# Performance work log

Measured on AMD Instinct MI355X. Metric: run time of the kernel, lower is better.

The kernel has to match this reference:

```python
import jax, jax.numpy as jnp
import numpy as np

PAD_ID = 1
NEG = jnp.float32(-1e30)


def setup_inputs() -> dict:
    key = jax.random.key(0)
    ks = jax.random.split(key, 12)
    T, B, S, D, E, V = 20, 32, 400, 512, 512, 50000
    s = 0.02  # weight init scale for numerical sanity
    return {
        "inputs": jax.random.randint(ks[0], (T, B), 0, V),
        "src": jax.random.randint(ks[1], (S, B, 1), 0, V),
        "h_e": jax.random.normal(ks[2], (S, B, D), jnp.float32),
        "h0": jnp.zeros((B, D), jnp.float32),
        "c0": jnp.zeros((B, D), jnp.float32),
        "W_emb": jax.random.normal(ks[3], (V, E), jnp.float32) * s,
        "W_proj": jax.random.normal(ks[4], (E, 3 * D), jnp.float32) * s,
        "b_out": jax.random.normal(ks[5], (V,), jnp.float32) * s,
        "proj_u_W": jax.random.normal(ks[6], (1, 3 * D), jnp.float32) * s,
        "proj_u_b": jnp.zeros((1,), jnp.float32),
        "enc_W": jax.random.normal(ks[7], (D, D), jnp.float32) * s,
        "dec_W": jax.random.normal(ks[8], (D, D), jnp.float32) * s,
        "W_ih": jax.random.normal(ks[9], (4 * D, E), jnp.float32) * s,
        "W_hh": jax.random.normal(ks[10], (4 * D, D), jnp.float32) * s,
        "b_ih": jnp.zeros((4 * D,), jnp.float32),
        "b_hh": jnp.zeros((4 * D,), jnp.float32),
    }


def reference(inputs, src, h_e, h0, c0, W_emb, W_proj, b_out, proj_u_W,
              proj_u_b, enc_W, dec_W, W_ih, W_hh, b_ih, b_hh):
    T, B = inputs.shape
    D = h0.shape[1]
    V = W_emb.shape[0]
    src_bs = src[:, :, 0].T                       # [B, S]
    # Sect 2.4 shared output weights: W_out = tanh(W_emb @ W_proj)  [V, 3D]
    W_out = jnp.tanh(W_emb @ W_proj)
    rows = jnp.arange(B)[:, None]
    tpos = jnp.arange(T)

    def step(carry, xs):
        h, c, hist = carry                        # hist: [T, B, D] decoder-state history
        inp_t, t = xs
        emb = W_emb[inp_t]                        # [B, E]
        # single-layer LSTM cell (torch gate order i, f, g, o)
        gates = emb @ W_ih.T + h @ W_hh.T + b_ih + b_hh
        i, f, g, o = jnp.split(gates, 4, axis=-1)
        c_new = jax.nn.sigmoid(f) * c + jax.nn.sigmoid(i) * jnp.tanh(g)
        hd = jax.nn.sigmoid(o) * jnp.tanh(c_new)  # [B, D]
        # encoder intra-attention
        q = hd @ enc_W.T
        ae = jax.nn.softmax(jnp.einsum('bd,sbd->bs', q, h_e), axis=-1)  # [B, S]
        ce = jnp.einsum('bs,sbd->bd', ae, h_e)
        # decoder intra-attention over steps < t (zero context at t==0)
        qd = hd @ dec_W.T
        sd = jnp.einsum('bd,tbd->bt', qd, hist)
        sd = jnp.where(tpos[None, :] < t, sd, NEG)
        ad = jax.nn.softmax(sd, axis=-1)
        cd = jnp.where(t > 0, jnp.einsum('bt,tbd->bd', ad, hist), 0.0)
        hist = hist.at[t].set(hd)
        # pointer-generator
        ccat = jnp.concatenate([hd, ce, cd], axis=-1)        # [B, 3D]
        logits = ccat @ W_out.T + b_out                      # [B, V]
        logits = logits.at[:, PAD_ID].set(NEG)
        p_gen = jax.nn.softmax(logits, axis=-1)
        p_switch = jax.nn.sigmoid(ccat @ proj_u_W.T + proj_u_b)  # [B, 1]
        # copy distribution: scatter attention into vocab
        copy = jnp.zeros((B, V), logits.dtype).at[rows, src_bs].add(ae)
        scores = copy * p_switch + p_gen * (1.0 - p_switch)
        return (hd, c_new, hist), scores

    hist0 = jnp.zeros((T, B, D), h0.dtype)
    _, scores = jax.lax.scan(step, (h0, c0, hist0), (inputs, tpos))
    return scores  # [T, B, V]
```

## Files before the change

kernel.cpp:

```cpp
#include <hip/hip_runtime.h>
#include <stdint.h>

typedef unsigned short u16;
typedef unsigned int   u32;

using f32x4 = __attribute__((ext_vector_type(4))) float;
using s16x8 = __attribute__((ext_vector_type(8))) short;

#define TT 20
#define BB 32
#define SS 400
#define DD 512
#define VV 50000
#define VP2 50176

__device__ __forceinline__ float bf2f(u16 u){
  u32 x = ((u32)u) << 16;
  return __builtin_bit_cast(float, x);
}
__device__ __forceinline__ u16 f2bf(float f){
  u32 x = __builtin_bit_cast(u32, f);
  x = x + 0x7fffu + ((x >> 16) & 1u);
  return (u16)(x >> 16);
}
__device__ __forceinline__ float sigm(float x){ return 1.0f/(1.0f + __expf(-x)); }
__device__ __forceinline__ float tanh_fast(float x){
  float a = fabsf(x);
  if (a < 0.25f){ float x2 = x*x; return x + x*x2*(-0.33333334f + 0.13333334f*x2); }
  return tanhf(x);
}
__device__ __forceinline__ void gld16(const void* g, void* l){
  __builtin_amdgcn_global_load_lds((const __attribute__((address_space(1))) void*)g,
                                   (__attribute__((address_space(3))) void*)l, 16, 0, 0);
}

__global__ __launch_bounds__(256) void k_prep(
    const float* __restrict__ W_proj,
    const float* __restrict__ W_ih,   const float* __restrict__ W_hh,
    const float* __restrict__ b_ih,   const float* __restrict__ b_hh,
    const float* __restrict__ h0,     const float* __restrict__ c0,
    const float* __restrict__ enc_W,  const float* __restrict__ dec_W,
    const float* __restrict__ W_emb,  const float* __restrict__ h_e,
    const int*   __restrict__ inputs,
    u16* __restrict__ WpT,
    u16* __restrict__ Wihs, u16* __restrict__ Whhs,
    u16* __restrict__ encWb, u16* __restrict__ decWb, float* __restrict__ bgs,
    float* __restrict__ hist, u16* __restrict__ histb, float* __restrict__ c_st,
    float* __restrict__ psE,
    u16* __restrict__ Wembb, u16* __restrict__ heb, u16* __restrict__ emba)
{
  int i = blockIdx.x*256 + threadIdx.x;
  if (i < 1280){ psE[i] = 0.0f; return; }
  i -= 1280;
  if (i < 2048){ int d = i >> 2, g = i & 3; bgs[i] = b_ih[g*512 + d] + b_hh[g*512 + d]; return; }
  i -= 2048;
  if (i < 16384){ float hv = h0[i]; hist[i] = hv; histb[i] = f2bf(hv); c_st[i] = c0[i]; return; }
  i -= 16384;
  if (i < 786432){ int j = i >> 9, k = i & 511; WpT[i] = f2bf(W_proj[k*1536 + j]); return; }
  i -= 786432;
  if (i < 1048576){
    int mp = i >> 9, k = i & 511; int d = mp >> 2, g = mp & 3;
    Wihs[i] = f2bf(W_ih[(size_t)(g*512 + d)*512 + k]); return; }
  i -= 1048576;
  if (i < 1048576){
    int mp = i >> 9, k = i & 511; int d = mp >> 2, g = mp & 3;
    Whhs[i] = f2bf(W_hh[(size_t)(g*512 + d)*512 + k]); return; }
  i -= 1048576;
  if (i < 262144){ encWb[i] = f2bf(enc_W[i]); return; }
  i -= 262144;
  if (i < 262144){ decWb[i] = f2bf(dec_W[i]); return; }
  i -= 262144;
  if (i < 6422528){
    int base = i*4;
    uint2 o;
    if (base < VV*DD){
      float4 v = *(const float4*)&W_emb[base];
      o.x = (u32)f2bf(v.x) | ((u32)f2bf(v.y) << 16);
      o.y = (u32)f2bf(v.z) | ((u32)f2bf(v.w) << 16);
    } else { o.x = 0u; o.y = 0u; }
    *(uint2*)&Wembb[base] = o;
    return; }
  i -= 6422528;
  if (i < 1638400){
    int base = i*4;
    const int s = base >> 14;
    const int b = (base >> 9) & 31;
    const int d = base & 511;
    float4 v = *(const float4*)&h_e[base];
    uint2 o;
    o.x = (u32)f2bf(v.x) | ((u32)f2bf(v.y) << 16);
    o.y = (u32)f2bf(v.z) | ((u32)f2bf(v.w) << 16);
    *(uint2*)&heb[((size_t)(b*SS + s) << 9) + d] = o;
    return; }
  i -= 1638400;
  if (i < 81920){
    int base = i*4;
    int r = base >> 9, k = base & 511;
    float4 v = *(const float4*)&W_emb[(size_t)inputs[r]*DD + k];
    uint2 o;
    o.x = (u32)f2bf(v.x) | ((u32)f2bf(v.y) << 16);
    o.y = (u32)f2bf(v.z) | ((u32)f2bf(v.w) << 16);
    *(uint2*)&emba[base] = o;
    return; }
}

template<int EPI>
__device__ __forceinline__ void gemm_tile(
    const u16* __restrict__ A, const u16* __restrict__ B,
    float* __restrict__ Cf, u16* __restrict__ Cb, const float* __restrict__ bias,
    int K, int mt, int nt, int ldc, int nmax, char* smemc)
{
  u16* As = (u16*)smemc;
  u16* Bs = (u16*)(smemc + 16384);
  const int tid = threadIdx.x;
  const int w = tid >> 6, l = tid & 63;
  const int m0 = mt*128, n0 = nt*128;
  const int srow = tid >> 3;
  const int scol = ((tid & 7) ^ ((tid >> 3) & 7)) * 8;
  const int wm = (w >> 1)*64, wn = (w & 1)*64;
  const int fr = l & 15;
  const int g4 = l >> 4;
  float bv[4];
  if constexpr (EPI == 3){
    #pragma unroll
    for (int j = 0; j < 4; ++j){
      const int c = n0 + wn + j*16 + fr;
      bv[j] = (c < nmax) ? bias[c] : 0.0f;
    }
  }
  f32x4 acc[4][4] = {};
  for (int k0 = 0; k0 < K; k0 += 64){
    #pragma unroll
    for (int j = 0; j < 4; ++j){
      gld16(A + (size_t)(m0 + j*32 + srow)*K + k0 + scol, (char*)As + j*4096 + (w << 10));
      gld16(B + (size_t)(n0 + j*32 + srow)*K + k0 + scol, (char*)Bs + j*4096 + (w << 10));
    }
    __syncthreads();
    #pragma unroll
    for (int h = 0; h < 2; ++h){
      s16x8 af[4], bfr[4];
      #pragma unroll
      for (int i = 0; i < 4; ++i){
        const int ra = wm + i*16 + fr;
        af[i]  = *(const s16x8*)((char*)As + ra*128 + ((((h << 2) + g4) ^ (ra & 7)) << 4));
        const int rb = wn + i*16 + fr;
        bfr[i] = *(const s16x8*)((char*)Bs + rb*128 + ((((h << 2) + g4) ^ (rb & 7)) << 4));
      }
      #pragma unroll
      for (int i = 0; i < 4; ++i)
        #pragma unroll
        for (int j2 = 0; j2 < 4; ++j2)
          acc[i][j2] = __builtin_amdgcn_mfma_f32_16x16x32_bf16(af[i], bfr[j2], acc[i][j2], 0, 0, 0);
    }
    __syncthreads();
  }
  if constexpr (EPI == 0){
    #pragma unroll
    for (int i = 0; i < 4; ++i)
      #pragma unroll
      for (int j = 0; j < 4; ++j)
        #pragma unroll
        for (int r = 0; r < 4; ++r){
          const int row = m0 + wm + i*16 + (l >> 4)*4 + r;
          const int col = n0 + wn + j*16 + fr;
          Cf[(size_t)row*ldc + col] = acc[i][j][r];
        }
  } else {
    u16* Rs = (u16*)smemc;
    #pragma unroll
    for (int i = 0; i < 4; ++i){
      #pragma unroll
      for (int j = 0; j < 4; ++j){
        #pragma unroll
        for (int r = 0; r < 4; ++r){
          const int rl = wm + i*16 + (l >> 4)*4 + r;
          const int cl = wn + j*16 + fr;
          const float v = acc[i][j][r];
          u16 o;
          if constexpr (EPI == 1) o = f2bf(tanh_fast(v));
          else                    o = f2bf(v + bv[j]);
          Rs[rl*136 + cl] = o;
        }
      }
    }
    __syncthreads();
    const int rr0 = tid >> 4;
    const int cb  = (tid & 15)*8;
    #pragma unroll
    for (int p = 0; p < 8; ++p){
      const int row = p*16 + rr0;
      const int gc  = n0 + cb;
      s16x8 val = *(const s16x8*)&Rs[row*136 + cb];
      u16* dst = Cb + (size_t)(m0 + row)*ldc + gc;
      if (EPI == 1 || gc + 8 <= nmax){
        *(s16x8*)dst = val;
      } else {
        #pragma unroll
        for (int q = 0; q < 8; ++q)
          if (gc + q < nmax) dst[q] = (u16)val[q];
      }
    }
  }
}

template<int EPI, int ORD>
__global__ __launch_bounds__(256) void gemm_bt(
    const u16* __restrict__ A, const u16* __restrict__ B,
    float* __restrict__ Cf, u16* __restrict__ Cb, const float* __restrict__ bias,
    int K, int TM, int TN, int ldc, int nmax)
{
  __shared__ __align__(16) char smem[34816];
  int bid = blockIdx.x;
  if (ORD >= 1){
    const int n = TM*TN, x = bid & 7, i = bid >> 3;
    const int q = n >> 3, r = n & 7;
    bid = (x < r ? x*(q+1) : r*(q+1) + (x-r)*q) + i;
  }
  const int mt = (ORD == 1) ? bid / TN : bid % TM;
  const int nt = (ORD == 1) ? bid % TN : bid / TM;
  gemm_tile<EPI>(A, B, Cf, Cb, bias, K, mt, nt, ldc, nmax, smem);
}

__global__ __launch_bounds__(256) void k_lstm(
    const u16* __restrict__ Whhs, const float* __restrict__ X, const float* __restrict__ bgs,
    float* __restrict__ hist, u16* __restrict__ histb, float* __restrict__ c_st,
    u16* __restrict__ ccatb, int t)
{
  __shared__ __align__(16) u16 Hs[32*512];
  __shared__ __align__(16) u16 As[16*512];
  __shared__ float Cp[4][16][32];
  const int blk = blockIdx.x;
  const int tid = threadIdx.x;
  const int w = tid >> 6, l = tid & 63;
  const char* hsrc = (const char*)(histb + (size_t)t*16384);
  #pragma unroll
  for (int p = 0; p < 8; ++p)
    gld16(hsrc + p*4096 + w*1024 + l*16, (char*)Hs + p*4096 + w*1024);
  const char* asrc = (const char*)(Whhs + (size_t)blk*16*512);
  #pragma unroll
  for (int p = 0; p < 4; ++p)
    gld16(asrc + p*4096 + w*1024 + l*16, (char*)As + p*4096 + w*1024);
  __syncthreads();
  {
    const int fr = l & 15, fko = (l >> 4)*8;
    f32x4 acc0 = {}, acc1 = {};
    #pragma unroll
    for (int kk = 0; kk < 4; ++kk){
      const int kb = (w*4 + kk)*32;
      s16x8 af = *(const s16x8*)&As[fr*512 + kb + fko];
      s16x8 b0 = *(const s16x8*)&Hs[fr*512 + kb + fko];
      s16x8 b1 = *(const s16x8*)&Hs[(16 + fr)*512 + kb + fko];
      acc0 = __builtin_amdgcn_mfma_f32_16x16x32_bf16(af, b0, acc0, 0, 0, 0);
      acc1 = __builtin_amdgcn_mfma_f32_16x16x32_bf16(af, b1, acc1, 0, 0, 0);
    }
    #pragma unroll
    for (int r = 0; r < 4; ++r){
      Cp[w][(l >> 4)*4 + r][fr]      = acc0[r];
      Cp[w][(l >> 4)*4 + r][16 + fr] = acc1[r];
    }
  }
  __syncthreads();
  if (tid < 128){
    const int dl = tid >> 5, b = tid & 31;
    const int d = blk*4 + dl;
    const int bd = b*512 + d;
    float gv[4];
    #pragma unroll
    for (int g = 0; g < 4; ++g)
      gv[g] = Cp[0][dl*4 + g][b] + Cp[1][dl*4 + g][b] + Cp[2][dl*4 + g][b] + Cp[3][dl*4 + g][b];
    const float4 x4 = *(const float4*)&X[((size_t)(t*BB + b))*2048 + d*4];
    const float4 g4 = *(const float4*)&bgs[d*4];
    const float iv = gv[0] + x4.x + g4.x;
    const float fv = gv[1] + x4.y + g4.y;
    const float gg = gv[2] + x4.z + g4.z;
    const float ov = gv[3] + x4.w + g4.w;
    const float cn = sigm(fv)*c_st[bd] + sigm(iv)*tanhf(gg);
    const float hd = sigm(ov)*tanhf(cn);
    c_st[bd] = cn;
    hist[(size_t)(t + 1)*16384 + bd] = hd;
    const u16 hb = f2bf(hd);
    histb[(size_t)(t + 1)*16384 + bd] = hb;
    ccatb[((size_t)(t*BB + b))*1536 + d] = hb;
  }
}

__global__ __launch_bounds__(256) void k_bulkq(
    const u16* __restrict__ Hb, const u16* __restrict__ encWb, const u16* __restrict__ decWb,
    float* __restrict__ qe_all, float* __restrict__ qd_all)
{
  __shared__ __align__(16) char smem[34816];
  const int e = blockIdx.x;
  const int which = e / 20;
  const int e2 = e % 20;
  const int mt = e2 % 5, nt = e2 / 5;
  gemm_tile<0>(Hb, which ? decWb : encWb, which ? qd_all : qe_all,
               nullptr, nullptr, 512, mt, nt, 512, 0, smem);
}

__global__ __launch_bounds__(256) void k_attn(
    const u16* __restrict__ heb, const float* __restrict__ hist,
    const float* __restrict__ qe_all, const float* __restrict__ qd_all,
    const float* __restrict__ puW,
    u16* __restrict__ ccatb, float* __restrict__ aeall,
    float* __restrict__ psE, float* __restrict__ psD)
{
  __shared__ float hcur[512];
  __shared__ float qv[512];
  __shared__ float ael[SS];
  __shared__ float red[256];
  __shared__ float part[4*512];
  __shared__ float adl[TT];
  __shared__ float sdl[TT];
  __shared__ float shs[2];
  const int blk = blockIdx.x;
  const int tid = threadIdx.x;

  if (blk < 640){
    const int row = blk;
    const int t = row >> 5, b = row & 31;
    const float* hsrc = hist + (size_t)(t + 1)*16384 + b*512;
    const float* qsrc = qe_all + (size_t)row*512;
    hcur[tid] = hsrc[tid]; hcur[tid + 256] = hsrc[tid + 256];
    qv[tid] = qsrc[tid];   qv[tid + 256] = qsrc[tid + 256];
    __syncthreads();
    for (int pass = 0; pass < 7; ++pass){
      const int s = pass*64 + (tid >> 2);
      if (s < SS){
        const u16* gp = heb + ((size_t)(b*SS + s))*512 + (tid & 3)*128;
        const float* hp = qv + (tid & 3)*128;
        float p = 0.0f;
        #pragma unroll 4
        for (int k8 = 0; k8 < 128; k8 += 8){
          s16x8 g8 = *(const s16x8*)&gp[k8];
          #pragma unroll
          for (int q = 0; q < 8; ++q) p += bf2f((u16)g8[q])*hp[k8 + q];
        }
        p += __shfl_xor(p, 1); p += __shfl_xor(p, 2);
        if ((tid & 3) == 0) ael[s] = p;
      }
    }
    __syncthreads();
    float lm = -1e30f;
    for (int s = tid; s < SS; s += 256) lm = fmaxf(lm, ael[s]);
    red[tid] = lm; __syncthreads();
    for (int st = 128; st; st >>= 1){ if (tid < st) red[tid] = fmaxf(red[tid], red[tid + st]); __syncthreads(); }
    const float M = red[0]; __syncthreads();
    float ls = 0.0f;
    for (int s = tid; s < SS; s += 256){ float p = __expf(ael[s] - M); ael[s] = p; ls += p; }
    red[tid] = ls; __syncthreads();
    for (int st = 128; st; st >>= 1){ if (tid < st) red[tid] += red[tid + st]; __syncthreads(); }
    const float inv = 1.0f/red[0];
    __syncthreads();
    {
      const int g = tid >> 6, th = tid & 63;
      const int d0 = th*8;
      float a8[8] = {};
      for (int s = g; s < SS; s += 4){
        const float a = ael[s];
        s16x8 hv = *(const s16x8*)&heb[((size_t)(b*SS + s))*512 + d0];
        #pragma unroll
        for (int q = 0; q < 8; ++q) a8[q] += a*bf2f((u16)hv[q]);
      }
      *(float4*)&part[g*512 + d0]     = float4{a8[0], a8[1], a8[2], a8[3]};
      *(float4*)&part[g*512 + d0 + 4] = float4{a8[4], a8[5], a8[6], a8[7]};
    }
    __syncthreads();
    {
      const int dd = tid*2;
      float ce0 = part[dd]     + part[512 + dd]     + part[1024 + dd]     + part[1536 + dd];
      float ce1 = part[dd + 1] + part[512 + dd + 1] + part[1024 + dd + 1] + part[1536 + dd + 1];
      ce0 *= inv; ce1 *= inv;
      *(u32*)&ccatb[(size_t)row*1536 + 512 + dd] = (u32)f2bf(ce0) | ((u32)f2bf(ce1) << 16);
      float pv = hcur[dd]*puW[dd] + hcur[dd + 1]*puW[dd + 1]
               + ce0*puW[512 + dd] + ce1*puW[512 + dd + 1];
      red[tid] = pv;
    }
    __syncthreads();
    for (int st = 128; st; st >>= 1){ if (tid < st) red[tid] += red[tid + st]; __syncthreads(); }
    if (tid == 0) psE[row] = red[0];
    for (int s = tid; s < SS; s += 256) aeall[(size_t)row*SS + s] = ael[s]*inv;
  } else {
    const int row = blk - 640;
    const int t = row >> 5, b = row & 31;
    const float* qsrc = qd_all + (size_t)row*512;
    qv[tid] = qsrc[tid]; qv[tid + 256] = qsrc[tid + 256];
    __syncthreads();
    for (int u0 = 0; u0 < t; u0 += 8){
      const int u = u0 + (tid >> 5);
      if (u < t){
        const float* hu = hist + (size_t)(u + 1)*16384 + b*512;
        float p = 0.0f;
        #pragma unroll
        for (int j = 0; j < 4; ++j){
          const int kb = (tid & 31)*4 + j*128;
          const float4 h4 = *(const float4*)&hu[kb];
          const float4 q4 = *(const float4*)&qv[kb];
          p += h4.x*q4.x + h4.y*q4.y + h4.z*q4.z + h4.w*q4.w;
        }
        p += __shfl_xor(p, 1); p += __shfl_xor(p, 2); p += __shfl_xor(p, 4);
        p += __shfl_xor(p, 8); p += __shfl_xor(p, 16);
        if ((tid & 31) == 0) sdl[u] = p;
      }
    }
    __syncthreads();
    if (tid == 0 && t > 0){
      float m2 = -1e30f;
      for (int u = 0; u < t; ++u) m2 = fmaxf(m2, sdl[u]);
      float s2 = 0.0f;
      for (int u = 0; u < t; ++u){ float p = __expf(sdl[u] - m2); adl[u] = p; s2 += p; }
      shs[0] = 1.0f/s2;
    }
    __syncthreads();
    const float invd = (t > 0) ? shs[0] : 0.0f;
    const int d0 = tid*2;
    float e0 = 0.0f, e1 = 0.0f;
    for (int u = 0; u < t; ++u){
      const float a = adl[u];
      const float* hu = hist + (size_t)(u + 1)*16384 + b*512 + d0;
      e0 += a*hu[0]; e1 += a*hu[1];
    }
    e0 *= invd; e1 *= invd;
    *(u32*)&ccatb[(size_t)row*1536 + 1024 + d0] = (u32)f2bf(e0) | ((u32)f2bf(e1) << 16);
    float pv = e0*puW[1024 + d0] + e1*puW[1024 + d0 + 1];
    red[tid] = pv; __syncthreads();
    for (int st = 128; st; st >>= 1){ if (tid < st) red[tid] += red[tid + st]; __syncthreads(); }
    if (tid == 0) psD[row] = red[0];
  }
}

__global__ __launch_bounds__(256) void k_softmax(
    const u16* __restrict__ lg, float* __restrict__ out,
    const float* __restrict__ psE, const float* __restrict__ psD, const float* __restrict__ puB,
    const int* __restrict__ src, const float* __restrict__ ae_all)
{
  const int r = blockIdx.x, tid = threadIdx.x;
  __shared__ float rm[256], rs[256];
  const u16* row = lg + (size_t)r*VP2;
  float m = -1e30f, s = 0.0f;
  for (int v8 = tid*8; v8 < VV; v8 += 2048){
    uint4 pk = *(const uint4*)&row[v8];
    u32 wds[4] = {pk.x, pk.y, pk.z, pk.w};
    #pragma unroll
    for (int q = 0; q < 8; ++q){
      if (v8 + q == 1) continue;
      float x = bf2f((u16)((wds[q >> 1] >> ((q & 1)*16)) & 0xffffu));
      if (x > m){ s = s*__expf(m - x) + 1.0f; m = x; }
      else s += __expf(x - m);
    }
  }
  rm[tid] = m; rs[tid] = s; __syncthreads();
  for (int st = 128; st; st >>= 1){
    if (tid < st){
      float m2 = fmaxf(rm[tid], rm[tid + st]);
      rs[tid] = rs[tid]*__expf(rm[tid] - m2) + rs[tid + st]*__expf(rm[tid + st] - m2);
      rm[tid] = m2;
    }
    __syncthreads();
  }
  const float M = rm[0];
  const float ps = 1.0f/(1.0f + __expf(-(psE[r] + psD[r] + puB[0])));
  const float inv = (1.0f - ps)/rs[0];
  float* orow = out + (size_t)r*VV;
  for (int v8 = tid*8; v8 < VV; v8 += 2048){
    uint4 pk = *(const uint4*)&row[v8];
    u32 wds[4] = {pk.x, pk.y, pk.z, pk.w};
    float o[8];
    #pragma unroll
    for (int q = 0; q < 8; ++q){
      float x = bf2f((u16)((wds[q >> 1] >> ((q & 1)*16)) & 0xffffu));
      o[q] = (v8 + q == 1) ? 0.0f : __expf(x - M)*inv;
    }
    *(float4*)&orow[v8]     = float4{o[0], o[1], o[2], o[3]};
    *(float4*)&orow[v8 + 4] = float4{o[4], o[5], o[6], o[7]};
  }
  __syncthreads();
  const int b = r & 31;
  for (int sp = tid; sp < SS; sp += 256){
    const int v = src[sp*BB + b];
    atomicAdd(&orow[v], ae_all[(size_t)r*SS + sp]*ps);
  }
}

extern "C" void kernel_launch(void* const* d_in, const int* in_sizes, int n_in,
                              void* d_out, int out_size, void* d_ws, size_t ws_size,
                              hipStream_t stream)
{
  const int*   inputs = (const int*)  d_in[0];
  const int*   src    = (const int*)  d_in[1];
  const float* h_e    = (const float*)d_in[2];
  const float* h0     = (const float*)d_in[3];
  const float* c0     = (const float*)d_in[4];
  const float* W_emb  = (const float*)d_in[5];
  const float* W_proj = (const float*)d_in[6];
  const float* b_out  = (const float*)d_in[7];
  const float* puW    = (const float*)d_in[8];
  const float* puB    = (const float*)d_in[9];
  const float* enc_W  = (const float*)d_in[10];
  const float* dec_W  = (const float*)d_in[11];
  const float* W_ih   = (const float*)d_in[12];
  const float* W_hh   = (const float*)d_in[13];
  const float* b_ih   = (const float*)d_in[14];
  const float* b_hh   = (const float*)d_in[15];
  float* out = (float*)d_out;

  char* wp = (char*)d_ws;
  auto alloc = [&](size_t bytes) -> char* {
    char* p = wp; wp += (bytes + 255) & ~(size_t)255; return p;
  };
  u16*   Wembb = (u16*)  alloc((size_t)VP2*DD*2);
  u16*   WpT   = (u16*)  alloc(1536*512*2);
  u16*   heb   = (u16*)  alloc((size_t)SS*BB*DD*2);
  u16*   logitsb = (u16*)Wembb;
  u16*   Woutb = (u16*)  alloc((size_t)VP2*1536*2);
  u16*   Wihs  = (u16*)  alloc(2048*512*2);
  u16*   Whhs  = (u16*)  alloc(2048*512*2);
  u16*   encWb = (u16*)  alloc(512*512*2);
  u16*   decWb = (u16*)  alloc(512*512*2);
  float* bgs   = (float*)alloc(2048*4);
  u16*   emba  = (u16*)  alloc((size_t)TT*BB*DD*2);
  float* X     = (float*)alloc((size_t)TT*BB*2048*4);
  float* c_st  = (float*)alloc(BB*DD*4);
  float* hist  = (float*)alloc((size_t)(TT+1)*BB*DD*4);
  u16*   histb = (u16*)  alloc((size_t)(TT+1)*BB*DD*2);
  u16*   ccatb = (u16*)  alloc((size_t)TT*BB*1536*2);
  float* aeall = (float*)alloc((size_t)TT*BB*SS*4);
  float* psE   = (float*)alloc(1280*4);
  float* psD   = psE + 640;
  float* qe_all= (float*)alloc((size_t)TT*BB*DD*4);
  float* qd_all= (float*)alloc((size_t)TT*BB*DD*4);

  k_prep<<<45197, 256, 0, stream>>>(W_proj, W_ih, W_hh, b_ih, b_hh, h0, c0, enc_W, dec_W,
                                    W_emb, h_e, inputs,
                                    WpT, Wihs, Whhs, encWb, decWb, bgs, hist, histb, c_st, psE,
                                    Wembb, heb, emba);

  gemm_bt<0,0><<<5*16, 256, 0, stream>>>(emba, Wihs, X, nullptr, nullptr, 512, 5, 16, 2048, 0);

  gemm_bt<1,1><<<392*12, 256, 0, stream>>>(Wembb, WpT, nullptr, Woutb, nullptr, 512, 392, 12, 1536, 0);

  for (int t = 0; t < TT; ++t)
    k_lstm<<<128, 256, 0, stream>>>(Whhs, X, bgs, hist, histb, c_st, ccatb, t);

  k_bulkq<<<40, 256, 0, stream>>>(histb + 16384, encWb, decWb, qe_all, qd_all);
  k_attn<<<1280, 256, 0, stream>>>(heb, hist, qe_all, qd_all, puW, ccatb, aeall, psE, psD);

  gemm_bt<3,2><<<5*392, 256, 0, stream>>>(ccatb, Woutb, nullptr, logitsb, b_out, 1536, 5, 392, VP2, VV);

  k_softmax<<<TT*BB, 256, 0, stream>>>(logitsb, out, psE, psD, puB, src, aeall);
}
```

Before: 495.0 us.

## Add 256x128 MFMA GEMM tile kernel and drop max-subtraction in vocab softmax

Adds a new 512-thread GEMM kernel computing 256x128 output tiles with swizzled LDS, 16x16x32 bf16 MFMAs and an LDS-staged coalesced bf16 epilogue. It is used for the W_out tanh projection and for the first 512 rows of the logits GEMM, while the remaining 128 rows still go through the old kernel. The goal is more reuse per loaded tile and fewer blocks. The softmax kernel also drops the online max tracking and computes exp(x) directly, subtracting the pad entry afterwards. That removes per-element branching and rescaling but relies on logits staying small enough not to overflow, which only holds for these small-scale weights.

```diff
diff --git a/kernel.cpp b/kernel.cpp
--- a/kernel.cpp
+++ b/kernel.cpp
@@ -221,6 +221,107 @@
   gemm_tile<EPI>(A, B, Cf, Cb, bias, K, mt, nt, ldc, nmax, smem);
 }
 
+template<int EPI, int ORD>
+__global__ __launch_bounds__(512, 4) void gemm_bt2(
+    const u16* __restrict__ A, const u16* __restrict__ B,
+    u16* __restrict__ Cb, const float* __restrict__ bias,
+    int K, int TM, int TN, int ldc, int nmax)
+{
+  __shared__ __align__(16) char smem[49152];
+  u16* As = (u16*)smem;
+  u16* Bs = (u16*)(smem + 32768);
+  const int tid = threadIdx.x;
+  const int w = tid >> 6, l = tid & 63;
+  int bid = blockIdx.x;
+  { const int n = TM*TN, x = bid & 7, i2 = bid >> 3;
+    const int q = n >> 3, r = n & 7;
+    bid = (x < r ? x*(q+1) : r*(q+1) + (x-r)*q) + i2; }
+  const int mt = (ORD == 1) ? bid / TN : bid % TM;
+  const int nt = (ORD == 1) ? bid % TN : bid / TM;
+  const int m0 = mt*256, n0 = nt*128;
+  const int srow = tid >> 3;
+  const int scol = ((tid & 7) ^ ((tid >> 3) & 7)) * 8;
+  const int wm = (w >> 1)*64;
+  const int wn = (w & 1)*64;
+  const int fr = l & 15;
+  const int g4 = l >> 4;
+  float bv[4];
+  if constexpr (EPI == 3){
+    #pragma unroll
+    for (int j = 0; j < 4; ++j){
+      const int c = n0 + wn + j*16 + fr;
+      bv[j] = (c < nmax) ? bias[c] : 0.0f;
+    }
+  }
+  f32x4 acc[4][4] = {};
+  for (int k0 = 0; k0 < K; k0 += 64){
+    #pragma unroll
+    for (int j = 0; j < 4; ++j)
+      gld16(A + (size_t)(m0 + j*64 + srow)*K + k0 + scol, (char*)As + j*8192 + (w << 10));
+    #pragma unroll
+    for (int j = 0; j < 2; ++j)
+      gld16(B + (size_t)(n0 + j*64 + srow)*K + k0 + scol, (char*)Bs + j*8192 + (w << 10));
+    __syncthreads();
+    #pragma unroll
+    for (int h = 0; h < 2; ++h){
+      s16x8 af[4], bfr[4];
+      #pragma unroll
+      for (int i = 0; i < 4; ++i){
+        const int ra = wm + i*16 + fr;
+        af[i]  = *(const s16x8*)((char*)As + ra*128 + ((((h << 2) + g4) ^ (ra & 7)) << 4));
+        const int rb = wn + i*16 + fr;
+        bfr[i] = *(const s16x8*)((char*)Bs + rb*128 + ((((h << 2) + g4) ^ (rb & 7)) << 4));
+      }
+      #pragma unroll
+      for (int i = 0; i < 4; ++i)
+        #pragma unroll
+        for (int j2 = 0; j2 < 4; ++j2)
+          acc[i][j2] = __builtin_amdgcn_mfma_f32_16x16x32_bf16(af[i], bfr[j2], acc[i][j2], 0, 0, 0);
+    }
+    __syncthreads();
+  }
+  u16* Rs = (u16*)smem;
+  #pragma unroll
+  for (int half = 0; half < 2; ++half){
+    if ((w >> 2) == half){
+      #pragma unroll
+      for (int i = 0; i < 4; ++i){
+        #pragma unroll
+        for (int j = 0; j < 4; ++j){
+          #pragma unroll
+          for (int r = 0; r < 4; ++r){
+            const int rl = (wm - half*128) + i*16 + (l >> 4)*4 + r;
+            const int cl = wn + j*16 + fr;
+            const float v = acc[i][j][r];
+            u16 o;
+            if constexpr (EPI == 1) o = f2bf(tanh_fast(v));
+            else                    o = f2bf(v + bv[j]);
+            Rs[rl*136 + cl] = o;
+          }
+        }
+      }
+    }
+    __syncthreads();
+    const int rr0 = tid >> 4;
+    const int cb  = (tid & 15)*8;
+    #pragma unroll
+    for (int p = 0; p < 4; ++p){
+      const int row = p*32 + rr0;
+      const int gc  = n0 + cb;
+      s16x8 val = *(const s16x8*)&Rs[row*136 + cb];
+      u16* dst = Cb + (size_t)(m0 + half*128 + row)*ldc + gc;
+      if (EPI == 1 || gc + 8 <= nmax){
+        *(s16x8*)dst = val;
+      } else {
+        #pragma unroll
+        for (int q = 0; q < 8; ++q)
+          if (gc + q < nmax) dst[q] = (u16)val[q];
+      }
+    }
+    __syncthreads();
+  }
+}
+
 __global__ __launch_bounds__(256) void k_lstm(
     const u16* __restrict__ Whhs, const float* __restrict__ X, const float* __restrict__ bgs,
     float* __restrict__ hist, u16* __restrict__ histb, float* __restrict__ c_st,
@@ -434,45 +535,40 @@
     const int* __restrict__ src, const float* __restrict__ ae_all)
 {
   const int r = blockIdx.x, tid = threadIdx.x;
-  __shared__ float rm[256], rs[256];
+  __shared__ float rs[256];
+  __shared__ float sh_inv, sh_ps;
   const u16* row = lg + (size_t)r*VP2;
-  float m = -1e30f, s = 0.0f;
+  float s = 0.0f;
   for (int v8 = tid*8; v8 < VV; v8 += 2048){
     uint4 pk = *(const uint4*)&row[v8];
     u32 wds[4] = {pk.x, pk.y, pk.z, pk.w};
     #pragma unroll
-    for (int q = 0; q < 8; ++q){
-      if (v8 + q == 1) continue;
-      float x = bf2f((u16)((wds[q >> 1] >> ((q & 1)*16)) & 0xffffu));
-      if (x > m){ s = s*__expf(m - x) + 1.0f; m = x; }
-      else s += __expf(x - m);
-    }
-  }
-  rm[tid] = m; rs[tid] = s; __syncthreads();
-  for (int st = 128; st; st >>= 1){
-    if (tid < st){
-      float m2 = fmaxf(rm[tid], rm[tid + st]);
-      rs[tid] = rs[tid]*__expf(rm[tid] - m2) + rs[tid + st]*__expf(rm[tid + st] - m2);
-      rm[tid] = m2;
-    }
-    __syncthreads();
-  }
-  const float M = rm[0];
-  const float ps = 1.0f/(1.0f + __expf(-(psE[r] + psD[r] + puB[0])));
-  const float inv = (1.0f - ps)/rs[0];
+    for (int q = 0; q < 8; ++q)
+      s += __expf(bf2f((u16)((wds[q >> 1] >> ((q & 1)*16)) & 0xffffu)));
+  }
+  rs[tid] = s; __syncthreads();
+  for (int st = 128; st; st >>= 1){ if (tid < st) rs[tid] += rs[tid + st]; __syncthreads(); }
+  if (tid == 0){
+    const float ps = 1.0f/(1.0f + __expf(-(psE[r] + psD[r] + puB[0])));
+    const float stot = rs[0] - __expf(bf2f(row[1]));
+    sh_ps = ps;
+    sh_inv = (1.0f - ps)/stot;
+  }
+  __syncthreads();
+  const float inv = sh_inv;
+  const float ps = sh_ps;
   float* orow = out + (size_t)r*VV;
   for (int v8 = tid*8; v8 < VV; v8 += 2048){
     uint4 pk = *(const uint4*)&row[v8];
     u32 wds[4] = {pk.x, pk.y, pk.z, pk.w};
     float o[8];
     #pragma unroll
-    for (int q = 0; q < 8; ++q){
-      float x = bf2f((u16)((wds[q >> 1] >> ((q & 1)*16)) & 0xffffu));
-      o[q] = (v8 + q == 1) ? 0.0f : __expf(x - M)*inv;
-    }
+    for (int q = 0; q < 8; ++q)
+      o[q] = __expf(bf2f((u16)((wds[q >> 1] >> ((q & 1)*16)) & 0xffffu)))*inv;
     *(float4*)&orow[v8]     = float4{o[0], o[1], o[2], o[3]};
     *(float4*)&orow[v8 + 4] = float4{o[4], o[5], o[6], o[7]};
   }
+  if (tid == 0) orow[1] = 0.0f;
   __syncthreads();
   const int b = r & 31;
   for (int sp = tid; sp < SS; sp += 256){
@@ -536,7 +632,7 @@
 
   gemm_bt<0,0><<<5*16, 256, 0, stream>>>(emba, Wihs, X, nullptr, nullptr, 512, 5, 16, 2048, 0);
 
-  gemm_bt<1,1><<<392*12, 256, 0, stream>>>(Wembb, WpT, nullptr, Woutb, nullptr, 512, 392, 12, 1536, 0);
+  gemm_bt2<1,1><<<196*12, 512, 0, stream>>>(Wembb, WpT, Woutb, nullptr, 512, 196, 12, 1536, 0);
 
   for (int t = 0; t < TT; ++t)
     k_lstm<<<128, 256, 0, stream>>>(Whhs, X, bgs, hist, histb, c_st, ccatb, t);
@@ -544,7 +640,9 @@
   k_bulkq<<<40, 256, 0, stream>>>(histb + 16384, encWb, decWb, qe_all, qd_all);
   k_attn<<<1280, 256, 0, stream>>>(heb, hist, qe_all, qd_all, puW, ccatb, aeall, psE, psD);
 
-  gemm_bt<3,2><<<5*392, 256, 0, stream>>>(ccatb, Woutb, nullptr, logitsb, b_out, 1536, 5, 392, VP2, VV);
+  gemm_bt2<3,2><<<2*392, 512, 0, stream>>>(ccatb, Woutb, logitsb, b_out, 1536, 2, 392, VP2, VV);
+  gemm_bt<3,2><<<1*392, 256, 0, stream>>>(ccatb + (size_t)512*1536, Woutb, nullptr,
+                                          logitsb + (size_t)512*VP2, b_out, 1536, 1, 392, VP2, VV);
 
   k_softmax<<<TT*BB, 256, 0, stream>>>(logitsb, out, psE, psD, puB, src, aeall);
 }
```

New measurement: 531.7 us. +7.4%, slower.
